# Optimization experiments

Measured on AMD Instinct MI355X. Metric: run time of the kernel, lower is better.

Reference implementation:

```python
import jax, jax.numpy as jnp
import numpy as np

BATCH, DIM, REPS = 4096, 2048, 8


def setup_inputs() -> dict:
    key = jax.random.key(0)
    ks = jax.random.split(key, 6)
    x = jax.random.normal(ks[0], (BATCH, DIM), jnp.float32)
    theta = 0.5 * jax.random.normal(ks[1], (DIM, REPS + 1, 2), jnp.float32)
    preacts_weight = 1.0 + 0.1 * jax.random.normal(ks[2], (DIM, REPS), jnp.float32)
    preacts_bias = 0.1 * jax.random.normal(ks[3], (DIM, REPS), jnp.float32)
    postact_weights = 1.0 + 0.1 * jax.random.normal(ks[4], (DIM,), jnp.float32)
    postact_bias = 0.1 * jax.random.normal(ks[5], (DIM,), jnp.float32)
    return dict(x=x, theta=theta, preacts_weight=preacts_weight,
                preacts_bias=preacts_bias, postact_weights=postact_weights,
                postact_bias=postact_bias)


def _rz(psi, ang):
    # RZ = diag(exp(-i*ang/2), exp(+i*ang/2)); ang broadcasts over (b, dim)
    ph = jnp.exp(ang * (-0.5j))  # complex64
    return jnp.stack([psi[..., 0] * ph, psi[..., 1] * jnp.conj(ph)], axis=-1)


def _ry(psi, ang):
    # RY = [[cos, -sin], [sin, cos]] with half-angle
    c = jnp.cos(0.5 * ang)
    s = jnp.sin(0.5 * ang)
    a, b = psi[..., 0], psi[..., 1]
    return jnp.stack([c * a - s * b, s * a + c * b], axis=-1)


def reference(x, theta, preacts_weight, preacts_bias, postact_weights, postact_bias):
    reps = theta.shape[1] - 1
    batch, dim = x.shape
    # encoded angles per rep: (reps, b, dim)
    enc = preacts_weight.T[:, None, :] * x[None] + preacts_bias.T[:, None, :]
    # |0> then Hadamard -> (1/sqrt2)(|0> + |1>) per (batch, dim) qubit
    inv_sqrt2 = jnp.asarray(1.0 / np.sqrt(2.0), jnp.complex64)
    psi0 = jnp.full((batch, dim, 2), inv_sqrt2, jnp.complex64)
    th0 = theta[:, :reps, 0].T  # (reps, dim)
    th1 = theta[:, :reps, 1].T  # (reps, dim)

    def step(psi, xs):
        t0, t1, e = xs
        psi = _rz(psi, t0)   # trainable RZ, (dim,) broadcast over batch
        psi = _ry(psi, t1)   # trainable RY
        psi = _rz(psi, e)    # data re-uploading RZ, (b, dim)
        return psi, None

    psi, _ = jax.lax.scan(step, psi0, (th0, th1, enc))
    psi = _rz(psi, theta[:, reps, 0])
    psi = _ry(psi, theta[:, reps, 1])
    # <Z> = |psi_0|^2 - |psi_1|^2, real float32
    z = (psi[..., 0].real ** 2 + psi[..., 0].imag ** 2) - \
        (psi[..., 1].real ** 2 + psi[..., 1].imag ** 2)
    return z * postact_weights + postact_bias
```

## Files before the change

kernel.cpp:

```cpp
#include <hip/hip_runtime.h>
#include <math.h>

constexpr int BATCH = 4096;
constexpr int DIM   = 2048;
constexpr int REPS  = 8;
constexpr float INV2PI = 0.15915494309189535f;

constexpr int TPB   = 256;
constexpr int GRIDX = DIM / TPB;
constexpr int GRIDY = 256;
constexpr int BPB   = BATCH / GRIDY;

__global__ __launch_bounds__(TPB, 4)
void daruan_kernel(const float* __restrict__ x,
                   const float* __restrict__ theta,
                   const float* __restrict__ paw,
                   const float* __restrict__ pab,
                   const float* __restrict__ postw,
                   const float* __restrict__ postb,
                   float* __restrict__ out)
{
    const int d = blockIdx.x * TPB + threadIdx.x;

    const float* th = theta + (size_t)d * 18;
    const float t00 = th[0] * INV2PI;
    const float X0  = __builtin_amdgcn_cosf(t00);
    const float Y0  = __builtin_amdgcn_sinf(t00);
    const float t10 = th[1] * INV2PI;
    const float Xi  = X0 * __builtin_amdgcn_cosf(t10);
    const float Yi  = Y0;
    const float Zi  = -X0 * __builtin_amdgcn_sinf(t10);

    float cy[REPS], sy[REPS], wr[REPS], br[REPS];
#pragma unroll
    for (int k = 0; k < REPS; ++k) {
        const float t1 = th[2 * k + 3] * INV2PI;
        cy[k] = __builtin_amdgcn_cosf(t1);
        sy[k] = __builtin_amdgcn_sinf(t1);
        wr[k] = paw[(size_t)d * REPS + k] * INV2PI;
        br[k] = (pab[(size_t)d * REPS + k] + th[2 * (k + 1)]) * INV2PI;
    }
    const float pw = postw[d];
    const float pb = postb[d];

    const int bbase = blockIdx.y * BPB;
    const float* xp = x + (size_t)bbase * DIM + d;
    float* op = out + (size_t)bbase * DIM + d;

    auto angles = [&](float xv, float (&se)[REPS], float (&ce)[REPS]) {
#pragma unroll
        for (int r = 0; r < REPS; ++r) {
            const float e = fmaf(wr[r], xv, br[r]);
            se[r] = __builtin_amdgcn_sinf(e);
            ce[r] = __builtin_amdgcn_cosf(e);
        }
    };
    auto state = [&](const float (&se)[REPS], const float (&ce)[REPS]) -> float {
        float X = fmaf(Xi, ce[0], -Yi * se[0]);
        float Y = fmaf(Xi, se[0],  Yi * ce[0]);
        float Z = Zi;
#pragma unroll
        for (int r = 1; r < REPS; ++r) {
            const float Xb = fmaf(X, cy[r - 1],  Z * sy[r - 1]);
            const float Zb = fmaf(Z, cy[r - 1], -X * sy[r - 1]);
            X = fmaf(Xb, ce[r], -Y * se[r]);
            if (r < REPS - 1)
                Y = fmaf(Xb, se[r], Y * ce[r]);
            Z = Zb;
        }
        return fmaf(Z, cy[REPS - 1], -X * sy[REPS - 1]);
    };

    float seA[REPS], ceA[REPS], seB[REPS], ceB[REPS];
    float x1;
    {
        const float xv0 = xp[0];
        angles(xv0, seA, ceA);
        x1 = xp[DIM];
    }

#pragma unroll 1
    for (int c = 0; c < BPB; c += 2) {
        angles(x1, seB, ceB);
        const float z0 = state(seA, ceA);
        op[(size_t)c * DIM] = fmaf(z0, pw, pb);
        const float xn0 = xp[(size_t)((c + 2) & (BPB - 1)) * DIM];
        angles(xn0, seA, ceA);
        const float z1 = state(seB, ceB);
        op[(size_t)(c + 1) * DIM] = fmaf(z1, pw, pb);
        x1 = xp[(size_t)((c + 3) & (BPB - 1)) * DIM];
    }
}

extern "C" void kernel_launch(void* const* d_in, const int* in_sizes, int n_in,
                              void* d_out, int out_size, void* d_ws, size_t ws_size,
                              hipStream_t stream) {
    const float* x     = (const float*)d_in[0];
    const float* theta = (const float*)d_in[1];
    const float* paw   = (const float*)d_in[2];
    const float* pab   = (const float*)d_in[3];
    const float* postw = (const float*)d_in[4];
    const float* postb = (const float*)d_in[5];
    float* out = (float*)d_out;

    daruan_kernel<<<dim3(GRIDX, GRIDY), dim3(TPB), 0, stream>>>(
        x, theta, paw, pab, postw, postb, out);
}
```

Before: 31.24 us.

## Split sincos between hardware transcendental unit and FMA polynomial, halve grid Y

Half of the data-reuploading angle sin/cos pairs are now evaluated with an FMA-based minimax polynomial after range reduction, while the other half still use the hardware sin/cos instructions. The goal is to balance work between the quarter-rate transcendental unit and the full-rate FMA pipe, which the transcendental unit had been bottlenecking. The grid Y dimension is also halved, so each block processes twice as many batch rows and the per-thread setup is amortized over more rows. The polynomial adds rounding error versus the hardware instructions and adds register pressure.

```diff
diff --git a/kernel.cpp b/kernel.cpp
--- a/kernel.cpp
+++ b/kernel.cpp
@@ -8,8 +8,23 @@
 
 constexpr int TPB   = 256;
 constexpr int GRIDX = DIM / TPB;
-constexpr int GRIDY = 256;
+constexpr int GRIDY = 128;
 constexpr int BPB   = BATCH / GRIDY;
+
+__device__ __forceinline__ void poly_sincos(float f, float& s, float& c) {
+    const float m = __builtin_rintf(f);
+    const float r = f - m;
+    const float u = r * r;
+    float p = fmaf(32.7680000f, u, -74.4701952f);
+    p = fmaf(p, u, 81.3660160f);
+    p = fmaf(p, u, -41.3311104f);
+    p = fmaf(p, u, 6.2830536f);
+    s = p * r;
+    float q = fmaf(45.6130560f, u, -82.3881728f);
+    q = fmaf(q, u, 64.6713088f);
+    q = fmaf(q, u, -19.7309120f);
+    c = fmaf(q, u, 0.9999527f);
+}
 
 __global__ __launch_bounds__(TPB, 4)
 void daruan_kernel(const float* __restrict__ x,
@@ -47,48 +62,53 @@
     const float* xp = x + (size_t)bbase * DIM + d;
     float* op = out + (size_t)bbase * DIM + d;
 
-    auto angles = [&](float xv, float (&se)[REPS], float (&ce)[REPS]) {
+    auto fill = [&](float xv, float (&seh)[4], float (&ceh)[4]) {
 #pragma unroll
-        for (int r = 0; r < REPS; ++r) {
-            const float e = fmaf(wr[r], xv, br[r]);
-            se[r] = __builtin_amdgcn_sinf(e);
-            ce[r] = __builtin_amdgcn_cosf(e);
+        for (int j = 0; j < 4; ++j) {
+            const float e = fmaf(wr[2 * j], xv, br[2 * j]);
+            seh[j] = __builtin_amdgcn_sinf(e);
+            ceh[j] = __builtin_amdgcn_cosf(e);
         }
     };
-    auto state = [&](const float (&se)[REPS], const float (&ce)[REPS]) -> float {
-        float X = fmaf(Xi, ce[0], -Yi * se[0]);
-        float Y = fmaf(Xi, se[0],  Yi * ce[0]);
+    auto consume = [&](float xv, const float (&seh)[4], const float (&ceh)[4]) -> float {
+        float sep[4], cep[4];
+#pragma unroll
+        for (int j = 0; j < 4; ++j)
+            poly_sincos(fmaf(wr[2 * j + 1], xv, br[2 * j + 1]), sep[j], cep[j]);
+
+        float X = fmaf(Xi, ceh[0], -Yi * seh[0]);
+        float Y = fmaf(Xi, seh[0],  Yi * ceh[0]);
         float Z = Zi;
 #pragma unroll
         for (int r = 1; r < REPS; ++r) {
+            const float se = (r & 1) ? sep[r >> 1] : seh[r >> 1];
+            const float ce = (r & 1) ? cep[r >> 1] : ceh[r >> 1];
             const float Xb = fmaf(X, cy[r - 1],  Z * sy[r - 1]);
             const float Zb = fmaf(Z, cy[r - 1], -X * sy[r - 1]);
-            X = fmaf(Xb, ce[r], -Y * se[r]);
+            X = fmaf(Xb, ce, -Y * se);
             if (r < REPS - 1)
-                Y = fmaf(Xb, se[r], Y * ce[r]);
+                Y = fmaf(Xb, se, Y * ce);
             Z = Zb;
         }
         return fmaf(Z, cy[REPS - 1], -X * sy[REPS - 1]);
     };
 
-    float seA[REPS], ceA[REPS], seB[REPS], ceB[REPS];
-    float x1;
-    {
-        const float xv0 = xp[0];
-        angles(xv0, seA, ceA);
-        x1 = xp[DIM];
-    }
+    float seA[4], ceA[4], seB[4], ceB[4];
+    float xA = xp[0];
+    fill(xA, seA, ceA);
+    float xB = xp[DIM];
 
 #pragma unroll 1
     for (int c = 0; c < BPB; c += 2) {
-        angles(x1, seB, ceB);
-        const float z0 = state(seA, ceA);
+        fill(xB, seB, ceB);
+        const float z0 = consume(xA, seA, ceA);
         op[(size_t)c * DIM] = fmaf(z0, pw, pb);
-        const float xn0 = xp[(size_t)((c + 2) & (BPB - 1)) * DIM];
-        angles(xn0, seA, ceA);
-        const float z1 = state(seB, ceB);
+        const float xn = xp[(size_t)((c + 2) & (BPB - 1)) * DIM];
+        fill(xn, seA, ceA);
+        const float z1 = consume(xB, seB, ceB);
         op[(size_t)(c + 1) * DIM] = fmaf(z1, pw, pb);
-        x1 = xp[(size_t)((c + 3) & (BPB - 1)) * DIM];
+        xA = xn;
+        xB = xp[(size_t)((c + 3) & (BPB - 1)) * DIM];
     }
 }
 
```

New measurement: 34.46 us. 10.3% more time.
